# Kernel optimization log

Measured on AMD Instinct MI355X. Metric: run time of the kernel, lower is better.

## Reference

```python
import jax, jax.numpy as jnp
import numpy as np

NUM_CLASSES = 10000
EMBED_LEN_DECODER = 100
DECODER_EMBEDDING = 768
DUPLICATE_FACTOR = int(NUM_CLASSES / EMBED_LEN_DECODER + 0.999)  # 100
BATCH = 512


def setup_inputs() -> dict:
    key = jax.random.key(0)
    k_h, k_w = jax.random.split(key)
    h = jax.random.normal(k_h, (BATCH, EMBED_LEN_DECODER, DECODER_EMBEDDING), dtype=jnp.float32)
    # xavier_normal over (decoder_embedding, duplicate_factor) fan dims
    std = (2.0 / (DECODER_EMBEDDING + DUPLICATE_FACTOR)) ** 0.5
    duplicate_pooling = std * jax.random.normal(
        k_w, (EMBED_LEN_DECODER, DECODER_EMBEDDING, DUPLICATE_FACTOR), dtype=jnp.float32)
    bias = jnp.zeros((NUM_CLASSES,), dtype=jnp.float32)
    return {"h": h, "duplicate_pooling": duplicate_pooling, "bias": bias}


def reference(h, duplicate_pooling, bias):
    # per-group batched matmul: out[b, i, f] = sum_d h[b, i, d] * W[i, d, f]
    out_extrap = jnp.einsum('bid,idf->bif', h, duplicate_pooling)
    # flatten groups, truncate to num_classes, add bias
    logits = out_extrap.reshape(h.shape[0], -1)[:, :NUM_CLASSES] + bias
    return logits
```

## Files before the change

### kernel.cpp

```cpp
#include <hip/hip_runtime.h>

typedef __attribute__((ext_vector_type(4))) float f32x4;
typedef __attribute__((ext_vector_type(8))) __bf16 bf16x8;
typedef __attribute__((ext_vector_type(8))) unsigned short ushort8v;

#define NGRP   100
#define DDIM   768
#define FDIM   100
#define NCLS   10000
#define NSTEP  12
#define NTILE  7
#define NCHUNK 14
#define CH_SHORTS 512
#define STEP_SHORTS (NCHUNK * CH_SHORTS)
#define G_SHORTS (NSTEP * STEP_SHORTS)

static __device__ __forceinline__ unsigned short f2bf(float f) {
    __bf16 b = (__bf16)f;
    return __builtin_bit_cast(unsigned short, b);
}

__global__ __launch_bounds__(256) void build_wt(
    const float* __restrict__ W, unsigned short* __restrict__ Wt)
{
    __shared__ unsigned short lt[FDIM * 66];
    const int b = blockIdx.x, g = b / 12, step = b % 12;
    const int tid = threadIdx.x;

    const float* Wg = W + (size_t)g * (DDIM * FDIM) + (size_t)step * 64 * FDIM;
#pragma unroll
    for (int j = 0; j < 25; ++j) {
        const int i = tid + j * 256;
        const int r = i / 100, f = i % 100;
        lt[f * 66 + r] = f2bf(Wg[i]);
    }
    __syncthreads();

    unsigned short* out = Wt + (size_t)g * G_SHORTS + step * STEP_SHORTS;
#pragma unroll
    for (int j = 0; j < 4; ++j) {
        const int idx = tid + j * 256;
        if (idx < NCHUNK * 64) {
            const int c = idx >> 6, lane = idx & 63;
            const int t = c >> 1, half = c & 1;
            int f = t * 16 + (lane & 15); if (f > FDIM - 1) f = FDIM - 1;
            const int kk = half * 32 + (lane >> 4) * 8;
            const unsigned short* src = &lt[f * 66 + kk];
            ushort8v v;
            v[0]=src[0]; v[1]=src[1]; v[2]=src[2]; v[3]=src[3];
            v[4]=src[4]; v[5]=src[5]; v[6]=src[6]; v[7]=src[7];
            *(ushort8v*)(out + (size_t)idx * 8) = v;
        }
    }
}

__global__ __launch_bounds__(64, 2) void gfcp_main(
    const float* __restrict__ H, const unsigned short* __restrict__ Wt,
    const float* __restrict__ Bv, float* __restrict__ Out)
{
    const int bid  = blockIdx.x;
    const int wgid = (bid & 7) * 400 + (bid >> 3);
    const int g    = wgid >> 5;
    const int m0   = (wgid & 31) * 16;

    const int lane = threadIdx.x & 63;
    const int r16  = lane & 15;
    const int kg   = lane >> 4;

    const float* Ap = H + (size_t)(m0 + r16) * (NGRP * DDIM)
                        + (size_t)g * DDIM + kg * 8;
    const unsigned short* Bg = Wt + (size_t)g * G_SHORTS + lane * 8;

    f32x4 acc[NTILE];
#pragma unroll
    for (int t = 0; t < NTILE; ++t) acc[t] = (f32x4)(0.0f);

    f32x4 a0[4], a1[4];
    ushort8v b0[NCHUNK], b1[NCHUNK];

#define LOADA(SL, STEP) do { \
        const float* p_ = Ap + (STEP) * 64; \
        SL[0] = *(const f32x4*)(p_); \
        SL[1] = *(const f32x4*)(p_ + 4); \
        SL[2] = *(const f32x4*)(p_ + 32); \
        SL[3] = *(const f32x4*)(p_ + 36); \
    } while (0)

#define LOADB(SL, STEP) do { \
        const unsigned short* q_ = Bg + (STEP) * STEP_SHORTS; \
        _Pragma("unroll") \
        for (int c_ = 0; c_ < NCHUNK; ++c_) \
            SL[c_] = *(const ushort8v*)(q_ + c_ * CH_SHORTS); \
    } while (0)

#define COMPUTE(ASL, BSL) do { \
        _Pragma("unroll") \
        for (int s_ = 0; s_ < 2; ++s_) { \
            ushort8v u_; \
            _Pragma("unroll") \
            for (int j_ = 0; j_ < 4; ++j_) { \
                u_[j_]     = f2bf(ASL[2*s_][j_]); \
                u_[j_ + 4] = f2bf(ASL[2*s_+1][j_]); \
            } \
            const bf16x8 af_ = __builtin_bit_cast(bf16x8, u_); \
            _Pragma("unroll") \
            for (int t_ = 0; t_ < NTILE; ++t_) { \
                acc[t_] = __builtin_amdgcn_mfma_f32_16x16x32_bf16( \
                    af_, __builtin_bit_cast(bf16x8, BSL[t_ * 2 + s_]), acc[t_], 0, 0, 0); \
            } \
        } \
    } while (0)

    LOADA(a0, 0);
    LOADA(a1, 1);
    LOADB(b0, 0);

#pragma unroll
    for (int t = 0; t < NSTEP; ++t) {
        if (t + 1 < NSTEP) {
            if ((t & 1) == 0) LOADB(b1, t + 1); else LOADB(b0, t + 1);
        }
        if ((t & 1) == 0) {
            COMPUTE(a0, b0);
            if (t + 2 < NSTEP) LOADA(a0, t + 2);
        } else {
            COMPUTE(a1, b1);
            if (t + 2 < NSTEP) LOADA(a1, t + 2);
        }
    }

    const int orow  = m0 + kg * 4;
    const int fbase = g * FDIM;
#pragma unroll
    for (int t = 0; t < NTILE; ++t) {
        const int fc = t * 16 + r16;
        if (fc < FDIM) {
            const float bv = Bv[fbase + fc];
#pragma unroll
            for (int r = 0; r < 4; ++r) {
                Out[(size_t)(orow + r) * NCLS + fbase + fc] = acc[t][r] + bv;
            }
        }
    }
}

extern "C" void kernel_launch(void* const* d_in, const int* in_sizes, int n_in,
                              void* d_out, int out_size, void* d_ws, size_t ws_size,
                              hipStream_t stream) {
    const float* H  = (const float*)d_in[0];
    const float* W  = (const float*)d_in[1];
    const float* Bv = (const float*)d_in[2];
    float* Out = (float*)d_out;
    unsigned short* Wt = (unsigned short*)d_ws;

    build_wt<<<dim3(1200), dim3(256), 0, stream>>>(W, Wt);
    gfcp_main<<<dim3(3200), dim3(64), 0, stream>>>(H, Wt, Bv, Out);
}
```

Measured before the change: 54.46 us.

## Split N tiles across four waves per block, add scheduling barriers

Each block now runs four waves that split the seven 16-wide output tiles (2,2,2,1) instead of one wave computing all seven. Every wave reloads and converts the same 16-row A slice, which multiplies global reads of H fourfold (served partly by cache) and duplicates the fp32-to-bf16 conversion. In exchange each wave needs fewer registers and has a shorter MFMA chain, which raises wave-level parallelism. Scheduling barriers are added to fix the order of loads and compute within each step. The load across the four waves is unbalanced because the last wave handles only one tile.

```diff
diff --git a/kernel.cpp b/kernel.cpp
--- a/kernel.cpp
+++ b/kernel.cpp
@@ -9,7 +9,6 @@
 #define FDIM   100
 #define NCLS   10000
 #define NSTEP  12
-#define NTILE  7
 #define NCHUNK 14
 #define CH_SHORTS 512
 #define STEP_SHORTS (NCHUNK * CH_SHORTS)
@@ -54,46 +53,36 @@
     }
 }
 
-__global__ __launch_bounds__(64, 2) void gfcp_main(
-    const float* __restrict__ H, const unsigned short* __restrict__ Wt,
-    const float* __restrict__ Bv, float* __restrict__ Out)
+template<int TB, int TCNT>
+__device__ __forceinline__ void wave_main(
+    const float* __restrict__ Ap, const unsigned short* __restrict__ Bg,
+    const float* __restrict__ Bv, float* __restrict__ Out,
+    int m0, int fbase, int lane)
 {
-    const int bid  = blockIdx.x;
-    const int wgid = (bid & 7) * 400 + (bid >> 3);
-    const int g    = wgid >> 5;
-    const int m0   = (wgid & 31) * 16;
+    const int r16 = lane & 15;
+    const int kg  = lane >> 4;
 
-    const int lane = threadIdx.x & 63;
-    const int r16  = lane & 15;
-    const int kg   = lane >> 4;
-
-    const float* Ap = H + (size_t)(m0 + r16) * (NGRP * DDIM)
-                        + (size_t)g * DDIM + kg * 8;
-    const unsigned short* Bg = Wt + (size_t)g * G_SHORTS + lane * 8;
-
-    f32x4 acc[NTILE];
+    f32x4 acc[TCNT];
 #pragma unroll
-    for (int t = 0; t < NTILE; ++t) acc[t] = (f32x4)(0.0f);
+    for (int t = 0; t < TCNT; ++t) acc[t] = (f32x4)(0.0f);
 
     f32x4 a0[4], a1[4];
-    ushort8v b0[NCHUNK], b1[NCHUNK];
+    ushort8v b0[2 * TCNT], b1[2 * TCNT];
 
-#define LOADA(SL, STEP) do { \
+#define LOADA_(SL, STEP) do { \
         const float* p_ = Ap + (STEP) * 64; \
         SL[0] = *(const f32x4*)(p_); \
         SL[1] = *(const f32x4*)(p_ + 4); \
         SL[2] = *(const f32x4*)(p_ + 32); \
         SL[3] = *(const f32x4*)(p_ + 36); \
     } while (0)
-
-#define LOADB(SL, STEP) do { \
-        const unsigned short* q_ = Bg + (STEP) * STEP_SHORTS; \
+#define LOADB_(SL, STEP) do { \
+        const unsigned short* q_ = Bg + (size_t)(STEP) * STEP_SHORTS; \
         _Pragma("unroll") \
-        for (int c_ = 0; c_ < NCHUNK; ++c_) \
-            SL[c_] = *(const ushort8v*)(q_ + c_ * CH_SHORTS); \
+        for (int c_ = 0; c_ < 2 * TCNT; ++c_) \
+            SL[c_] = *(const ushort8v*)(q_ + (2 * TB + c_) * CH_SHORTS); \
     } while (0)
-
-#define COMPUTE(ASL, BSL) do { \
+#define COMPUTE_(ASL, BSL) do { \
         _Pragma("unroll") \
         for (int s_ = 0; s_ < 2; ++s_) { \
             ushort8v u_; \
@@ -104,44 +93,68 @@
             } \
             const bf16x8 af_ = __builtin_bit_cast(bf16x8, u_); \
             _Pragma("unroll") \
-            for (int t_ = 0; t_ < NTILE; ++t_) { \
+            for (int t_ = 0; t_ < TCNT; ++t_) \
                 acc[t_] = __builtin_amdgcn_mfma_f32_16x16x32_bf16( \
-                    af_, __builtin_bit_cast(bf16x8, BSL[t_ * 2 + s_]), acc[t_], 0, 0, 0); \
-            } \
+                    af_, __builtin_bit_cast(bf16x8, BSL[t_*2 + s_]), acc[t_], 0, 0, 0); \
         } \
     } while (0)
 
-    LOADA(a0, 0);
-    LOADA(a1, 1);
-    LOADB(b0, 0);
+    LOADA_(a0, 0);
+    LOADA_(a1, 1);
+    LOADB_(b0, 0);
+    __builtin_amdgcn_sched_barrier(0);
 
 #pragma unroll
     for (int t = 0; t < NSTEP; ++t) {
         if (t + 1 < NSTEP) {
-            if ((t & 1) == 0) LOADB(b1, t + 1); else LOADB(b0, t + 1);
+            if ((t & 1) == 0) LOADB_(b1, t + 1); else LOADB_(b0, t + 1);
+            __builtin_amdgcn_sched_barrier(0);
         }
-        if ((t & 1) == 0) {
-            COMPUTE(a0, b0);
-            if (t + 2 < NSTEP) LOADA(a0, t + 2);
-        } else {
-            COMPUTE(a1, b1);
-            if (t + 2 < NSTEP) LOADA(a1, t + 2);
-        }
+        if ((t & 1) == 0) { COMPUTE_(a0, b0); if (t + 2 < NSTEP) LOADA_(a0, t + 2); }
+        else              { COMPUTE_(a1, b1); if (t + 2 < NSTEP) LOADA_(a1, t + 2); }
+        __builtin_amdgcn_sched_barrier(0);
     }
+#undef LOADA_
+#undef LOADB_
+#undef COMPUTE_
 
-    const int orow  = m0 + kg * 4;
-    const int fbase = g * FDIM;
+    const int orow = m0 + kg * 4;
 #pragma unroll
-    for (int t = 0; t < NTILE; ++t) {
-        const int fc = t * 16 + r16;
+    for (int tt = 0; tt < TCNT; ++tt) {
+        const int fc = (TB + tt) * 16 + r16;
         if (fc < FDIM) {
             const float bv = Bv[fbase + fc];
 #pragma unroll
-            for (int r = 0; r < 4; ++r) {
-                Out[(size_t)(orow + r) * NCLS + fbase + fc] = acc[t][r] + bv;
-            }
+            for (int r = 0; r < 4; ++r)
+                Out[(size_t)(orow + r) * NCLS + fbase + fc] = acc[tt][r] + bv;
         }
     }
+}
+
+__global__ __launch_bounds__(256, 4) void gfcp_main(
+    const float* __restrict__ H, const unsigned short* __restrict__ Wt,
+    const float* __restrict__ Bv, float* __restrict__ Out)
+{
+    const int bid  = blockIdx.x;
+    const int wgid = (bid & 7) * 400 + (bid >> 3);
+    const int g    = wgid >> 5;
+    const int m0   = (wgid & 31) * 16;
+
+    const int tid  = threadIdx.x;
+    const int lane = tid & 63;
+    const int wv   = tid >> 6;
+    const int r16  = lane & 15;
+    const int kg   = lane >> 4;
+
+    const float* Ap = H + (size_t)(m0 + r16) * (NGRP * DDIM)
+                        + (size_t)g * DDIM + kg * 8;
+    const unsigned short* Bg = Wt + (size_t)g * G_SHORTS + lane * 8;
+    const int fbase = g * FDIM;
+
+    if      (wv == 0) wave_main<0, 2>(Ap, Bg, Bv, Out, m0, fbase, lane);
+    else if (wv == 1) wave_main<2, 2>(Ap, Bg, Bv, Out, m0, fbase, lane);
+    else if (wv == 2) wave_main<4, 2>(Ap, Bg, Bv, Out, m0, fbase, lane);
+    else              wave_main<6, 1>(Ap, Bg, Bv, Out, m0, fbase, lane);
 }
 
 extern "C" void kernel_launch(void* const* d_in, const int* in_sizes, int n_in,
@@ -154,5 +167,5 @@
     unsigned short* Wt = (unsigned short*)d_ws;
 
     build_wt<<<dim3(1200), dim3(256), 0, stream>>>(W, Wt);
-    gfcp_main<<<dim3(3200), dim3(64), 0, stream>>>(H, Wt, Bv, Out);
+    gfcp_main<<<dim3(3200), dim3(256), 0, stream>>>(H, Wt, Bv, Out);
 }
```

After: 100.0 us. +83.6%, slower.
